# Optimization experiments

Hardware: AMD Instinct MI355X
Metric: run time of the kernel (lower is better)

The kernel has to match this reference:

```python
import jax, jax.numpy as jnp
import numpy as np

N_NODES = 100000
NUM_APS = 1000
K = 2
IN_F = 32
HID = 64


def _glorot(key, shape):
    fan_in, fan_out = shape[-2], shape[-1]
    lim = (6.0 / (fan_in + fan_out)) ** 0.5
    return jax.random.uniform(key, shape, jnp.float32, -lim, lim)


def setup_inputs() -> dict:
    key = jax.random.key(0)
    ks = jax.random.split(key, 12)
    x = jax.random.normal(ks[0], (N_NODES, IN_F), jnp.float32)
    edge_index = jax.random.randint(ks[1], (2, 1600000), 0, N_NODES, jnp.int32)
    edge_attr = jax.random.uniform(ks[2], (1600000, 1), jnp.float32)
    # TAGConv1: K+1 weight matrices [in, hid] + bias
    w1 = _glorot(ks[3], (K + 1, IN_F, HID))
    b1 = jnp.zeros((HID,), jnp.float32)
    # TAGConv2: K+1 weight matrices [hid, hid] + bias
    w2 = _glorot(ks[4], (K + 1, HID, HID))
    b2 = jnp.zeros((HID,), jnp.float32)
    wch = _glorot(ks[5], (HID, 3))
    bch = jnp.zeros((3,), jnp.float32)
    wpw = _glorot(ks[6], (HID, 3))
    bpw = jnp.zeros((3,), jnp.float32)
    return {"x": x, "edge_index": edge_index, "edge_attr": edge_attr,
            "w1": w1, "b1": b1, "w2": w2, "b2": b2,
            "wch": wch, "bch": bch, "wpw": wpw, "bpw": bpw}


def _gcn_norm(edge_index, edge_weight, num_nodes):
    # PyG gcn_norm with add_self_loops=False (TAGConv default)
    row, col = edge_index[0], edge_index[1]
    deg = jax.ops.segment_sum(edge_weight, col, num_segments=num_nodes)
    dinv = jnp.where(deg > 0, deg ** -0.5, 0.0)
    return dinv[row] * edge_weight * dinv[col]


def _tagconv(x, edge_index, norm, w, b):
    # out = sum_k lin_k(A_hat^k x) + b
    row, col = edge_index[0], edge_index[1]
    out = x @ w[0]
    h = x
    for k in range(1, w.shape[0]):
        msg = h[row] * norm[:, None]              # [E, F] gather + scale
        h = jax.ops.segment_sum(msg, col, num_segments=x.shape[0])
        out = out + h @ w[k]
    return out + b


def reference(x, edge_index, edge_attr, w1, b1, w2, b2, wch, bch, wpw, bpw):
    edge_weight = edge_attr.squeeze()
    norm = _gcn_norm(edge_index, edge_weight, x.shape[0])
    h = jax.nn.leaky_relu(_tagconv(x, edge_index, norm, w1, b1), 0.01)
    h = jax.nn.leaky_relu(_tagconv(h, edge_index, norm, w2, b2), 0.01)
    ap = h[:NUM_APS]
    channel_logits = ap @ wch + bch
    power_logits = ap @ wpw + bpw
    return (channel_logits, power_logits)
```

## Files before the change

kernel.cpp:

```cpp
#include <hip/hip_runtime.h>
#include <hip/hip_bf16.h>

#define N_NODES 100000
#define NUM_APS 1000
#define IN_F 32
#define HID 64
#define NB 391
#define EPB 4096
#define CAPB 4608
#define LISTCAP 24000
#define ZERON 100513

typedef __hip_bfloat16 bf16;
typedef unsigned long long ull;
typedef __attribute__((ext_vector_type(8))) short bf16x8;
typedef __attribute__((ext_vector_type(4))) float f32x4;

__device__ __forceinline__ float b2f(bf16 v) { return __bfloat162float(v); }
__device__ __forceinline__ float blo(unsigned u) { return __uint_as_float(u << 16); }
__device__ __forceinline__ float bhi(unsigned u) { return __uint_as_float(u & 0xffff0000u); }
__device__ __forceinline__ unsigned packbf(float x, float y) {
    bf16 a = __float2bfloat16(x), b = __float2bfloat16(y);
    unsigned short ua = *reinterpret_cast<unsigned short*>(&a);
    unsigned short ub = *reinterpret_cast<unsigned short*>(&b);
    return (unsigned)ua | ((unsigned)ub << 16);
}
__device__ __forceinline__ short f2bs(float v) {
    bf16 t = __float2bfloat16(v);
    return *reinterpret_cast<short*>(&t);
}
__device__ __forceinline__ unsigned rec_r(unsigned v) { return v >> 15; }
__device__ __forceinline__ float rec_w(unsigned v) { return (v & 32767u) * (1.f / 32768.f); }

__global__ void zero_k(int* __restrict__ p) {
    int i = blockIdx.x * 256 + threadIdx.x;
    if (i < ZERON) p[i] = 0;
}

__global__ __launch_bounds__(512) void binwrite2_k(const int* __restrict__ row,
                                                   const int* __restrict__ col,
                                                   const float* __restrict__ ew,
                                                   int* __restrict__ binPtr,
                                                   ull* __restrict__ staging, int E) {
    __shared__ int h1[NB];
    __shared__ int base[NB];
    __shared__ int h2[NB];
    for (int i = threadIdx.x; i < NB; i += 512) { h1[i] = 0; h2[i] = 0; }
    __syncthreads();
    int e0 = blockIdx.x * EPB, e1 = min(e0 + EPB, E);
    for (int e = e0 + threadIdx.x; e < e1; e += 512) atomicAdd(&h1[col[e] >> 8], 1);
    __syncthreads();
    for (int i = threadIdx.x; i < NB; i += 512) {
        int v = h1[i];
        base[i] = v ? atomicAdd(&binPtr[i], v) : 0;
    }
    __syncthreads();
    for (int e = e0 + threadIdx.x; e < e1; e += 512) {
        int c = col[e];
        int b = c >> 8;
        int slot = atomicAdd(&h2[b], 1);
        unsigned q = (unsigned)(ew[e] * 32768.0f + 0.5f);
        if (q > 32767u) q = 32767u;
        ull rec = ((ull)(unsigned)(c & 255) << 32) |
                  (ull)(((unsigned)row[e] << 15) | q);
        int pos = base[b] + slot;
        if (pos < CAPB) staging[(size_t)b * CAPB + pos] = rec;
    }
}

__global__ __launch_bounds__(512) void binscan2_k(const int* __restrict__ binPtr,
                                                  int* __restrict__ binBase) {
    __shared__ int s[512];
    int v = (threadIdx.x < NB) ? min(binPtr[threadIdx.x], CAPB) : 0;
    s[threadIdx.x] = v;
    __syncthreads();
    for (int d = 1; d < 512; d <<= 1) {
        int t = (threadIdx.x >= d) ? s[threadIdx.x - d] : 0;
        __syncthreads();
        s[threadIdx.x] += t;
        __syncthreads();
    }
    if (threadIdx.x <= NB) binBase[threadIdx.x] = s[threadIdx.x] - v;
}

__global__ __launch_bounds__(256) void binfin2x_k(const ull* __restrict__ staging,
                                                  const int* __restrict__ binBase,
                                                  const float* __restrict__ x,
                                                  unsigned* __restrict__ ed,
                                                  int* __restrict__ off,
                                                  float* __restrict__ dinv,
                                                  unsigned* __restrict__ xs) {
    __shared__ unsigned cnt[256];
    __shared__ unsigned degq[256];
    __shared__ int wptr[256];
    __shared__ unsigned s[256];
    __shared__ float sdv[256];
    int b = blockIdx.x;
    int e0 = binBase[b];
    int cntb = binBase[b + 1] - e0;
    const ull* st = staging + (size_t)b * CAPB;
    cnt[threadIdx.x] = 0;
    degq[threadIdx.x] = 0;
    __syncthreads();
    for (int i = threadIdx.x; i < cntb; i += 256) {
        ull rec = st[i];
        unsigned cl = (unsigned)(rec >> 32) & 255u;
        atomicAdd(&cnt[cl], 1u);
        atomicAdd(&degq[cl], (unsigned)rec & 32767u);
    }
    __syncthreads();
    unsigned v = cnt[threadIdx.x];
    s[threadIdx.x] = v;
    __syncthreads();
    for (int d = 1; d < 256; d <<= 1) {
        unsigned t = (threadIdx.x >= d) ? s[threadIdx.x - d] : 0;
        __syncthreads();
        s[threadIdx.x] += t;
        __syncthreads();
    }
    int colg = (b << 8) + threadIdx.x;
    float dv = 0.f;
    if (colg < N_NODES) {
        off[colg] = e0 + (int)s[threadIdx.x];
        float deg = (float)degq[threadIdx.x] * (1.0f / 32768.0f);
        dv = deg > 0.f ? 1.0f / sqrtf(deg) : 0.f;
        dinv[colg] = dv;
    }
    sdv[threadIdx.x] = dv;
    wptr[threadIdx.x] = e0 + (int)s[threadIdx.x] - (int)v;
    __syncthreads();
    for (int i = threadIdx.x; i < cntb; i += 256) {
        ull rec = st[i];
        unsigned cl = (unsigned)(rec >> 32) & 255u;
        int pos = atomicAdd(&wptr[cl], 1);
        ed[pos] = (unsigned)rec;
    }
    int nb0 = b << 8;
    for (int idx = threadIdx.x; idx < 256 * 16; idx += 256) {
        int n = idx >> 4, c = idx & 15;
        int gn = nb0 + n;
        if (gn >= N_NODES) break;
        float d = sdv[n];
        xs[(size_t)gn * 16 + c] = packbf(x[(size_t)gn * 32 + 2 * c] * d,
                                         x[(size_t)gn * 32 + 2 * c + 1] * d);
    }
}

__global__ __launch_bounds__(256) void activeset_k(const unsigned* __restrict__ ed,
                                                   const int* __restrict__ off,
                                                   int* __restrict__ mark,
                                                   int* __restrict__ list,
                                                   int* __restrict__ cnt) {
    int e = blockIdx.x * 256 + threadIdx.x;
    int end = off[NUM_APS - 1];
    if (e >= end) return;
    int r = (int)rec_r(ed[e]);
    if (atomicExch(&mark[r], 1) == 0) {
        int pos = atomicAdd(cnt, 1);
        if (pos < LISTCAP) list[pos] = r;
    }
}

__global__ __launch_bounds__(256) void gath32_dual_k(const unsigned* __restrict__ ed,
                                                     const int* __restrict__ off,
                                                     const float* __restrict__ dinv,
                                                     const uint4* __restrict__ src4,
                                                     uint4* __restrict__ p4,
                                                     uint4* __restrict__ u4, int nn) {
    int t = blockIdx.x * 256 + threadIdx.x;
    int n = t >> 2;
    if (n >= nn) return;
    int qd = t & 3;
    int s = (n == 0) ? 0 : off[n - 1];
    int e = off[n];
    float aA[8] = {0,0,0,0,0,0,0,0};
    float aB[8] = {0,0,0,0,0,0,0,0};
    float aC[8] = {0,0,0,0,0,0,0,0};
    float aD[8] = {0,0,0,0,0,0,0,0};
    int i = s;
    for (; i + 4 <= e; i += 4) {
        unsigned v0 = ed[i], v1 = ed[i + 1], v2 = ed[i + 2], v3 = ed[i + 3];
        uint4 s0 = src4[rec_r(v0) * 4 + qd];
        uint4 s1 = src4[rec_r(v1) * 4 + qd];
        uint4 s2 = src4[rec_r(v2) * 4 + qd];
        uint4 s3 = src4[rec_r(v3) * 4 + qd];
        float w0 = rec_w(v0), w1 = rec_w(v1), w2 = rec_w(v2), w3 = rec_w(v3);
        aA[0] += w0 * blo(s0.x); aA[1] += w0 * bhi(s0.x);
        aA[2] += w0 * blo(s0.y); aA[3] += w0 * bhi(s0.y);
        aA[4] += w0 * blo(s0.z); aA[5] += w0 * bhi(s0.z);
        aA[6] += w0 * blo(s0.w); aA[7] += w0 * bhi(s0.w);
        aB[0] += w1 * blo(s1.x); aB[1] += w1 * bhi(s1.x);
        aB[2] += w1 * blo(s1.y); aB[3] += w1 * bhi(s1.y);
        aB[4] += w1 * blo(s1.z); aB[5] += w1 * bhi(s1.z);
        aB[6] += w1 * blo(s1.w); aB[7] += w1 * bhi(s1.w);
        aC[0] += w2 * blo(s2.x); aC[1] += w2 * bhi(s2.x);
        aC[2] += w2 * blo(s2.y); aC[3] += w2 * bhi(s2.y);
        aC[4] += w2 * blo(s2.z); aC[5] += w2 * bhi(s2.z);
        aC[6] += w2 * blo(s2.w); aC[7] += w2 * bhi(s2.w);
        aD[0] += w3 * blo(s3.x); aD[1] += w3 * bhi(s3.x);
        aD[2] += w3 * blo(s3.y); aD[3] += w3 * bhi(s3.y);
        aD[4] += w3 * blo(s3.z); aD[5] += w3 * bhi(s3.z);
        aD[6] += w3 * blo(s3.w); aD[7] += w3 * bhi(s3.w);
    }
    for (; i < e; ++i) {
        unsigned v = ed[i];
        uint4 sv = src4[rec_r(v) * 4 + qd];
        float w = rec_w(v);
        aA[0] += w * blo(sv.x); aA[1] += w * bhi(sv.x);
        aA[2] += w * blo(sv.y); aA[3] += w * bhi(sv.y);
        aA[4] += w * blo(sv.z); aA[5] += w * bhi(sv.z);
        aA[6] += w * blo(sv.w); aA[7] += w * bhi(sv.w);
    }
#pragma unroll
    for (int k = 0; k < 8; ++k) aA[k] += aB[k] + aC[k] + aD[k];
    float d = dinv[n], d2 = d * d;
    p4[n * 4 + qd] = make_uint4(packbf(d * aA[0], d * aA[1]), packbf(d * aA[2], d * aA[3]),
                                packbf(d * aA[4], d * aA[5]), packbf(d * aA[6], d * aA[7]));
    u4[n * 4 + qd] = make_uint4(packbf(d2 * aA[0], d2 * aA[1]), packbf(d2 * aA[2], d2 * aA[3]),
                                packbf(d2 * aA[4], d2 * aA[5]), packbf(d2 * aA[6], d2 * aA[7]));
}

__global__ __launch_bounds__(256) void gath32_one_k(const unsigned* __restrict__ ed,
                                                    const int* __restrict__ off,
                                                    const float* __restrict__ dinv,
                                                    const uint4* __restrict__ src4,
                                                    uint4* __restrict__ p4, int nn) {
    int t = blockIdx.x * 256 + threadIdx.x;
    int n = t >> 2;
    if (n >= nn) return;
    int qd = t & 3;
    int s = (n == 0) ? 0 : off[n - 1];
    int e = off[n];
    float aA[8] = {0,0,0,0,0,0,0,0};
    float aB[8] = {0,0,0,0,0,0,0,0};
    float aC[8] = {0,0,0,0,0,0,0,0};
    float aD[8] = {0,0,0,0,0,0,0,0};
    int i = s;
    for (; i + 4 <= e; i += 4) {
        unsigned v0 = ed[i], v1 = ed[i + 1], v2 = ed[i + 2], v3 = ed[i + 3];
        uint4 s0 = src4[rec_r(v0) * 4 + qd];
        uint4 s1 = src4[rec_r(v1) * 4 + qd];
        uint4 s2 = src4[rec_r(v2) * 4 + qd];
        uint4 s3 = src4[rec_r(v3) * 4 + qd];
        float w0 = rec_w(v0), w1 = rec_w(v1), w2 = rec_w(v2), w3 = rec_w(v3);
        aA[0] += w0 * blo(s0.x); aA[1] += w0 * bhi(s0.x);
        aA[2] += w0 * blo(s0.y); aA[3] += w0 * bhi(s0.y);
        aA[4] += w0 * blo(s0.z); aA[5] += w0 * bhi(s0.z);
        aA[6] += w0 * blo(s0.w); aA[7] += w0 * bhi(s0.w);
        aB[0] += w1 * blo(s1.x); aB[1] += w1 * bhi(s1.x);
        aB[2] += w1 * blo(s1.y); aB[3] += w1 * bhi(s1.y);
        aB[4] += w1 * blo(s1.z); aB[5] += w1 * bhi(s1.z);
        aB[6] += w1 * blo(s1.w); aB[7] += w1 * bhi(s1.w);
        aC[0] += w2 * blo(s2.x); aC[1] += w2 * bhi(s2.x);
        aC[2] += w2 * blo(s2.y); aC[3] += w2 * bhi(s2.y);
        aC[4] += w2 * blo(s2.z); aC[5] += w2 * bhi(s2.z);
        aC[6] += w2 * blo(s2.w); aC[7] += w2 * bhi(s2.w);
        aD[0] += w3 * blo(s3.x); aD[1] += w3 * bhi(s3.x);
        aD[2] += w3 * blo(s3.y); aD[3] += w3 * bhi(s3.y);
        aD[4] += w3 * blo(s3.z); aD[5] += w3 * bhi(s3.z);
        aD[6] += w3 * blo(s3.w); aD[7] += w3 * bhi(s3.w);
    }
    for (; i < e; ++i) {
        unsigned v = ed[i];
        uint4 sv = src4[rec_r(v) * 4 + qd];
        float w = rec_w(v);
        aA[0] += w * blo(sv.x); aA[1] += w * bhi(sv.x);
        aA[2] += w * blo(sv.y); aA[3] += w * bhi(sv.y);
        aA[4] += w * blo(sv.z); aA[5] += w * bhi(sv.z);
        aA[6] += w * blo(sv.w); aA[7] += w * bhi(sv.w);
    }
#pragma unroll
    for (int k = 0; k < 8; ++k) aA[k] += aB[k] + aC[k] + aD[k];
    float d = dinv[n];
    p4[n * 4 + qd] = make_uint4(packbf(d * aA[0], d * aA[1]), packbf(d * aA[2], d * aA[3]),
                                packbf(d * aA[4], d * aA[5]), packbf(d * aA[6], d * aA[7]));
}

__global__ __launch_bounds__(256) void gath64_l2_k(const unsigned* __restrict__ ed,
                                                   const int* __restrict__ off,
                                                   const float* __restrict__ dinv,
                                                   const unsigned* __restrict__ src,
                                                   const int* __restrict__ list,
                                                   const int* __restrict__ cnt,
                                                   unsigned* __restrict__ u,
                                                   unsigned* __restrict__ q) {
    int t = blockIdx.x * 256 + threadIdx.x;
    int idx = t >> 5;
    int fp = t & 31;
    int n;
    bool wq;
    if (idx < NUM_APS) {
        n = idx;
        wq = true;
    } else {
        int j = idx - NUM_APS;
        int c = *cnt;
        if (c > LISTCAP) c = LISTCAP;
        if (j >= c) return;
        n = list[j];
        wq = false;
    }
    int s = (n == 0) ? 0 : off[n - 1];
    int e = off[n];
    float a0 = 0.f, a1 = 0.f, b0 = 0.f, b1 = 0.f;
    int i = s;
    for (; i + 4 <= e; i += 4) {
        unsigned v0 = ed[i], v1 = ed[i + 1], v2 = ed[i + 2], v3 = ed[i + 3];
        unsigned s0 = src[rec_r(v0) * 32 + fp];
        unsigned s1 = src[rec_r(v1) * 32 + fp];
        unsigned s2 = src[rec_r(v2) * 32 + fp];
        unsigned s3 = src[rec_r(v3) * 32 + fp];
        float w0 = rec_w(v0), w1 = rec_w(v1), w2 = rec_w(v2), w3 = rec_w(v3);
        a0 += w0 * blo(s0); a1 += w0 * bhi(s0);
        b0 += w1 * blo(s1); b1 += w1 * bhi(s1);
        a0 += w2 * blo(s2); a1 += w2 * bhi(s2);
        b0 += w3 * blo(s3); b1 += w3 * bhi(s3);
    }
    for (; i < e; ++i) {
        unsigned v = ed[i];
        unsigned sv = src[rec_r(v) * 32 + fp];
        float w = rec_w(v);
        a0 += w * blo(sv); a1 += w * bhi(sv);
    }
    a0 += b0; a1 += b1;
    float d = dinv[n], d2 = d * d;
    u[n * 32 + fp] = packbf(d2 * a0, d2 * a1);
    if (wq) q[n * 32 + fp] = packbf(d * a0, d * a1);
}

__global__ __launch_bounds__(256) void gath64_one_k(const unsigned* __restrict__ ed,
                                                    const int* __restrict__ off,
                                                    const float* __restrict__ dinv,
                                                    const unsigned* __restrict__ src,
                                                    unsigned* __restrict__ q, int nn) {
    int t = blockIdx.x * 256 + threadIdx.x;
    int n = t >> 5;
    if (n >= nn) return;
    int fp = t & 31;
    int s = (n == 0) ? 0 : off[n - 1];
    int e = off[n];
    float a0 = 0.f, a1 = 0.f, b0 = 0.f, b1 = 0.f;
    int i = s;
    for (; i + 4 <= e; i += 4) {
        unsigned v0 = ed[i], v1 = ed[i + 1], v2 = ed[i + 2], v3 = ed[i + 3];
        unsigned s0 = src[rec_r(v0) * 32 + fp];
        unsigned s1 = src[rec_r(v1) * 32 + fp];
        unsigned s2 = src[rec_r(v2) * 32 + fp];
        unsigned s3 = src[rec_r(v3) * 32 + fp];
        float w0 = rec_w(v0), w1 = rec_w(v1), w2 = rec_w(v2), w3 = rec_w(v3);
        a0 += w0 * blo(s0); a1 += w0 * bhi(s0);
        b0 += w1 * blo(s1); b1 += w1 * bhi(s1);
        a0 += w2 * blo(s2); a1 += w2 * bhi(s2);
        b0 += w3 * blo(s3); b1 += w3 * bhi(s3);
    }
    for (; i < e; ++i) {
        unsigned v = ed[i];
        unsigned sv = src[rec_r(v) * 32 + fp];
        float w = rec_w(v);
        a0 += w * blo(sv); a1 += w * bhi(sv);
    }
    a0 += b0; a1 += b1;
    float d = dinv[n];
    q[n * 32 + fp] = packbf(d * a0, d * a1);
}

__global__ __launch_bounds__(256) void dense1m_k(const float* __restrict__ x,
                                                 const unsigned* __restrict__ p1,
                                                 const unsigned* __restrict__ p2,
                                                 const float* __restrict__ w,
                                                 const float* __restrict__ b,
                                                 const float* __restrict__ dinv,
                                                 bf16* __restrict__ h1s,
                                                 bf16* __restrict__ h1p) {
    __shared__ short sxb[64 * 104];
    __shared__ short swt[64 * 104];
    __shared__ float sbias[64];
    __shared__ float sdv[64];
    int tid = threadIdx.x;
    int nb = blockIdx.x * 64;
    for (int idx = tid; idx < 96 * 64; idx += 256) {
        int j = idx >> 6, f = idx & 63;
        swt[f * 104 + j] = f2bs(w[idx]);
    }
    for (int i = tid; i < 64 * 16; i += 256) {
        int n = i >> 4, c = i & 15;
        int gn = nb + n;
        float v0 = 0.f, v1 = 0.f;
        if (gn < N_NODES) {
            v0 = x[(size_t)gn * 32 + 2 * c];
            v1 = x[(size_t)gn * 32 + 2 * c + 1];
        }
        ((unsigned*)sxb)[n * 52 + c] = packbf(v0, v1);
    }
    for (int i = tid; i < 64 * 16; i += 256) {
        int n = i >> 4, c = i & 15;
        int gn = nb + n;
        unsigned v1 = 0u, v2 = 0u;
        if (gn < N_NODES) {
            v1 = p1[(size_t)gn * 16 + c];
            v2 = p2[(size_t)gn * 16 + c];
        }
        ((unsigned*)sxb)[n * 52 + 16 + c] = v1;
        ((unsigned*)sxb)[n * 52 + 32 + c] = v2;
    }
    if (tid < 64) {
        sbias[tid] = b[tid];
        int gn = nb + tid;
        sdv[tid] = (gn < N_NODES) ? dinv[gn] : 0.f;
    }
    __syncthreads();

    int lane = tid & 63;
    int wt = tid >> 6;
    int lr = lane & 15;
    int kg = lane >> 4;
    const short* arow = &sxb[(wt * 16 + lr) * 104 + kg * 8];
    bf16x8 a0 = *(const bf16x8*)(arow);
    bf16x8 a1 = *(const bf16x8*)(arow + 32);
    bf16x8 a2 = *(const bf16x8*)(arow + 64);
#pragma unroll
    for (int ct = 0; ct < 4; ++ct) {
        const short* bcol = &swt[(ct * 16 + lr) * 104 + kg * 8];
        bf16x8 b0 = *(const bf16x8*)(bcol);
        bf16x8 b1 = *(const bf16x8*)(bcol + 32);
        bf16x8 b2 = *(const bf16x8*)(bcol + 64);
        f32x4 acc = {0.f, 0.f, 0.f, 0.f};
        acc = __builtin_amdgcn_mfma_f32_16x16x32_bf16(a0, b0, acc, 0, 0, 0);
        acc = __builtin_amdgcn_mfma_f32_16x16x32_bf16(a1, b1, acc, 0, 0, 0);
        acc = __builtin_amdgcn_mfma_f32_16x16x32_bf16(a2, b2, acc, 0, 0, 0);
        int colo = ct * 16 + lr;
        float bias = sbias[colo];
#pragma unroll
        for (int r = 0; r < 4; ++r) {
            int rowl = wt * 16 + kg * 4 + r;
            int gn = nb + rowl;
            if (gn < N_NODES) {
                float a = acc[r] + bias;
                a = a > 0.f ? a : 0.01f * a;
                h1s[(size_t)gn * HID + colo] = __float2bfloat16(a * sdv[rowl]);
                if (gn < NUM_APS) h1p[(size_t)gn * HID + colo] = __float2bfloat16(a);
            }
        }
    }
}

__global__ __launch_bounds__(256) void dense2l_k(const bf16* __restrict__ h1p,
                                                 const bf16* __restrict__ q1,
                                                 const bf16* __restrict__ q2,
                                                 const float* __restrict__ w,
                                                 const float* __restrict__ b,
                                                 const float* __restrict__ wch,
                                                 const float* __restrict__ bch,
                                                 const float* __restrict__ wpw,
                                                 const float* __restrict__ bpw,
                                                 float* __restrict__ out) {
    __shared__ float sw[3 * HID * HID];
    __shared__ float sx[4][3 * HID];
    __shared__ float sap[4][HID];
    for (int i = threadIdx.x; i < 3 * HID * HID; i += 256) sw[i] = w[i];
    int nb = blockIdx.x * 4;
    for (int k = threadIdx.x; k < 4 * 192; k += 256) {
        int ln = k / 192, j = k % 192;
        int n = nb + ln;
        float v = 0.f;
        if (n < NUM_APS) {
            int hop = j >> 6, ii = j & 63;
            const bf16* sp = (hop == 0) ? h1p : (hop == 1 ? q1 : q2);
            v = b2f(sp[n * HID + ii]);
        }
        sx[ln][j] = v;
    }
    __syncthreads();
    int ln = threadIdx.x >> 6;
    int f = threadIdx.x & 63;
    float acc = b[f];
#pragma unroll 8
    for (int j = 0; j < 192; ++j) acc += sx[ln][j] * sw[j * HID + f];
    acc = acc > 0.f ? acc : 0.01f * acc;
    sap[ln][f] = acc;
    __syncthreads();
    if (threadIdx.x < 24) {
        int lnn = threadIdx.x / 6, j = threadIdx.x % 6;
        int n = nb + lnn;
        if (n < NUM_APS) {
            const float* wp;
            float bb;
            float* o;
            if (j < 3) {
                wp = wch + j; bb = bch[j]; o = out + n * 3 + j;
            } else {
                int jj = j - 3;
                wp = wpw + jj; bb = bpw[jj]; o = out + NUM_APS * 3 + n * 3 + jj;
            }
            float a = bb;
#pragma unroll
            for (int i = 0; i < HID; ++i) a += sap[lnn][i] * wp[i * 3];
            *o = a;
        }
    }
}

extern "C" void kernel_launch(void* const* d_in, const int* in_sizes, int n_in,
                              void* d_out, int out_size, void* d_ws, size_t ws_size,
                              hipStream_t stream) {
    const float* x   = (const float*)d_in[0];
    const int*   ei  = (const int*)d_in[1];
    const float* ea  = (const float*)d_in[2];
    const float* w1  = (const float*)d_in[3];
    const float* b1  = (const float*)d_in[4];
    const float* w2  = (const float*)d_in[5];
    const float* b2  = (const float*)d_in[6];
    const float* wch = (const float*)d_in[7];
    const float* bch = (const float*)d_in[8];
    const float* wpw = (const float*)d_in[9];
    const float* bpw = (const float*)d_in[10];

    const int E = in_sizes[2];
    const int* row  = ei;
    const int* colv = ei + E;

    float* ws = (float*)d_ws;
    ull*      staging = (ull*)ws;
    unsigned* ed      = (unsigned*)(ws + 3700000);
    int*      binPtr  = (int*)(ws + 5300000);
    int*      acnt    = (int*)(ws + 5300512);
    int*      mark    = (int*)(ws + 5300513);
    int*      binBase = (int*)(ws + 5401024);
    int*      off     = (int*)(ws + 5402048);
    float*    dinv    = ws + 5502048;
    unsigned* xs      = (unsigned*)(ws + 5602048);
    unsigned* u1      = xs + 1600000;
    unsigned* p1      = (unsigned*)(ws + 8802048);
    unsigned* p2      = p1 + 1600000;
    unsigned* h1s     = xs;
    unsigned* u3      = p1;
    bf16*     h1p     = (bf16*)(ws + 12002048);
    bf16*     q1      = (bf16*)(ws + 12034048);
    bf16*     q2      = (bf16*)(ws + 12066048);
    int*      alist   = (int*)(ws + 12098048);

    const int gridE = (E + EPB - 1) / EPB;

    zero_k<<<(ZERON + 255) / 256, 256, 0, stream>>>(binPtr);

    binwrite2_k<<<gridE, 512, 0, stream>>>(row, colv, ea, binPtr, staging, E);
    binscan2_k<<<1, 512, 0, stream>>>(binPtr, binBase);
    binfin2x_k<<<NB, 256, 0, stream>>>(staging, binBase, x, ed, off, dinv, xs);

    activeset_k<<<128, 256, 0, stream>>>(ed, off, mark, alist, acnt);

    gath32_dual_k<<<(N_NODES * 4 + 255) / 256, 256, 0, stream>>>(ed, off, dinv,
                                                                 (const uint4*)xs,
                                                                 (uint4*)p1, (uint4*)u1,
                                                                 N_NODES);
    gath32_one_k<<<(N_NODES * 4 + 255) / 256, 256, 0, stream>>>(ed, off, dinv,
                                                                (const uint4*)u1,
                                                                (uint4*)p2, N_NODES);
    dense1m_k<<<(N_NODES + 63) / 64, 256, 0, stream>>>(x, p1, p2, w1, b1, dinv,
                                                       (bf16*)h1s, h1p);

    gath64_l2_k<<<((NUM_APS + LISTCAP) * 32 + 255) / 256, 256, 0, stream>>>(
        ed, off, dinv, h1s, alist, acnt, u3, (unsigned*)q1);
    gath64_one_k<<<(NUM_APS * 32 + 255) / 256, 256, 0, stream>>>(ed, off, dinv, u3,
                                                                 (unsigned*)q2, NUM_APS);
    dense2l_k<<<(NUM_APS + 3) / 4, 256, 0, stream>>>(h1p, q1, q2, w2, b2,
                                                     wch, bch, wpw, bpw, (float*)d_out);
}
```

Baseline: 148.4 us.

## Fuse bin scan, active-set and final gather kernels to cut launches

Removes the single-block bin scan by having each finalize block compute its own prefix offset with a reduction over bin counts. It folds the active-set marking into extra blocks of the first 32-wide gather kernel. It also merges the last hop-2 gather into the final dense kernel. Together these remove three kernel launches and the serialization between them, at the cost of redundant prefix work in every block and a serial per-edge gather loop inside the dense kernel.

```diff
diff --git a/kernel.cpp b/kernel.cpp
--- a/kernel.cpp
+++ b/kernel.cpp
@@ -10,6 +10,8 @@
 #define CAPB 4608
 #define LISTCAP 24000
 #define ZERON 100513
+#define G32 ((N_NODES * 4 + 255) / 256)
+#define ACTB 128
 
 typedef __hip_bfloat16 bf16;
 typedef unsigned long long ull;
@@ -68,75 +70,74 @@
     }
 }
 
-__global__ __launch_bounds__(512) void binscan2_k(const int* __restrict__ binPtr,
-                                                  int* __restrict__ binBase) {
-    __shared__ int s[512];
-    int v = (threadIdx.x < NB) ? min(binPtr[threadIdx.x], CAPB) : 0;
-    s[threadIdx.x] = v;
-    __syncthreads();
-    for (int d = 1; d < 512; d <<= 1) {
-        int t = (threadIdx.x >= d) ? s[threadIdx.x - d] : 0;
-        __syncthreads();
-        s[threadIdx.x] += t;
-        __syncthreads();
-    }
-    if (threadIdx.x <= NB) binBase[threadIdx.x] = s[threadIdx.x] - v;
-}
-
-__global__ __launch_bounds__(256) void binfin2x_k(const ull* __restrict__ staging,
-                                                  const int* __restrict__ binBase,
-                                                  const float* __restrict__ x,
-                                                  unsigned* __restrict__ ed,
-                                                  int* __restrict__ off,
-                                                  float* __restrict__ dinv,
-                                                  unsigned* __restrict__ xs) {
+__global__ __launch_bounds__(256) void binfin3_k(const ull* __restrict__ staging,
+                                                 const int* __restrict__ binPtr,
+                                                 const float* __restrict__ x,
+                                                 unsigned* __restrict__ ed,
+                                                 int* __restrict__ off,
+                                                 float* __restrict__ dinv,
+                                                 unsigned* __restrict__ xs) {
+    __shared__ int sbp[NB];
     __shared__ unsigned cnt[256];
     __shared__ unsigned degq[256];
     __shared__ int wptr[256];
     __shared__ unsigned s[256];
     __shared__ float sdv[256];
+    __shared__ int se0;
     int b = blockIdx.x;
-    int e0 = binBase[b];
-    int cntb = binBase[b + 1] - e0;
+    int tid = threadIdx.x;
+    for (int i = tid; i < NB; i += 256) sbp[i] = min(binPtr[i], CAPB);
+    cnt[tid] = 0;
+    degq[tid] = 0;
+    __syncthreads();
+    int partial = 0;
+    for (int i = tid; i < b; i += 256) partial += sbp[i];
+    s[tid] = (unsigned)partial;
+    __syncthreads();
+    for (int d = 128; d > 0; d >>= 1) {
+        if (tid < d) s[tid] += s[tid + d];
+        __syncthreads();
+    }
+    if (tid == 0) se0 = (int)s[0];
+    __syncthreads();
+    int e0 = se0;
+    int cntb = sbp[b];
     const ull* st = staging + (size_t)b * CAPB;
-    cnt[threadIdx.x] = 0;
-    degq[threadIdx.x] = 0;
-    __syncthreads();
-    for (int i = threadIdx.x; i < cntb; i += 256) {
+    for (int i = tid; i < cntb; i += 256) {
         ull rec = st[i];
         unsigned cl = (unsigned)(rec >> 32) & 255u;
         atomicAdd(&cnt[cl], 1u);
         atomicAdd(&degq[cl], (unsigned)rec & 32767u);
     }
     __syncthreads();
-    unsigned v = cnt[threadIdx.x];
-    s[threadIdx.x] = v;
+    unsigned v = cnt[tid];
+    s[tid] = v;
     __syncthreads();
     for (int d = 1; d < 256; d <<= 1) {
-        unsigned t = (threadIdx.x >= d) ? s[threadIdx.x - d] : 0;
+        unsigned t = (tid >= d) ? s[tid - d] : 0;
         __syncthreads();
-        s[threadIdx.x] += t;
+        s[tid] += t;
         __syncthreads();
     }
-    int colg = (b << 8) + threadIdx.x;
+    int colg = (b << 8) + tid;
     float dv = 0.f;
     if (colg < N_NODES) {
-        off[colg] = e0 + (int)s[threadIdx.x];
-        float deg = (float)degq[threadIdx.x] * (1.0f / 32768.0f);
+        off[colg] = e0 + (int)s[tid];
+        float deg = (float)degq[tid] * (1.0f / 32768.0f);
         dv = deg > 0.f ? 1.0f / sqrtf(deg) : 0.f;
         dinv[colg] = dv;
     }
-    sdv[threadIdx.x] = dv;
-    wptr[threadIdx.x] = e0 + (int)s[threadIdx.x] - (int)v;
-    __syncthreads();
-    for (int i = threadIdx.x; i < cntb; i += 256) {
+    sdv[tid] = dv;
+    wptr[tid] = e0 + (int)s[tid] - (int)v;
+    __syncthreads();
+    for (int i = tid; i < cntb; i += 256) {
         ull rec = st[i];
         unsigned cl = (unsigned)(rec >> 32) & 255u;
         int pos = atomicAdd(&wptr[cl], 1);
         ed[pos] = (unsigned)rec;
     }
     int nb0 = b << 8;
-    for (int idx = threadIdx.x; idx < 256 * 16; idx += 256) {
+    for (int idx = tid; idx < 256 * 16; idx += 256) {
         int n = idx >> 4, c = idx & 15;
         int gn = nb0 + n;
         if (gn >= N_NODES) break;
@@ -146,30 +147,30 @@
     }
 }
 
-__global__ __launch_bounds__(256) void activeset_k(const unsigned* __restrict__ ed,
-                                                   const int* __restrict__ off,
-                                                   int* __restrict__ mark,
-                                                   int* __restrict__ list,
-                                                   int* __restrict__ cnt) {
-    int e = blockIdx.x * 256 + threadIdx.x;
-    int end = off[NUM_APS - 1];
-    if (e >= end) return;
-    int r = (int)rec_r(ed[e]);
-    if (atomicExch(&mark[r], 1) == 0) {
-        int pos = atomicAdd(cnt, 1);
-        if (pos < LISTCAP) list[pos] = r;
-    }
-}
-
-__global__ __launch_bounds__(256) void gath32_dual_k(const unsigned* __restrict__ ed,
-                                                     const int* __restrict__ off,
-                                                     const float* __restrict__ dinv,
-                                                     const uint4* __restrict__ src4,
-                                                     uint4* __restrict__ p4,
-                                                     uint4* __restrict__ u4, int nn) {
+__global__ __launch_bounds__(256) void gath32a_k(const unsigned* __restrict__ ed,
+                                                 const int* __restrict__ off,
+                                                 const float* __restrict__ dinv,
+                                                 const uint4* __restrict__ src4,
+                                                 uint4* __restrict__ p4,
+                                                 uint4* __restrict__ u4,
+                                                 int* __restrict__ mark,
+                                                 int* __restrict__ list,
+                                                 int* __restrict__ cnt) {
+    if (blockIdx.x >= G32) {
+        int e = (blockIdx.x - G32) * 256 + threadIdx.x;
+        int end = off[NUM_APS - 1];
+        if (e < end) {
+            int r = (int)rec_r(ed[e]);
+            if (atomicExch(&mark[r], 1) == 0) {
+                int pos = atomicAdd(cnt, 1);
+                if (pos < LISTCAP) list[pos] = r;
+            }
+        }
+        return;
+    }
     int t = blockIdx.x * 256 + threadIdx.x;
     int n = t >> 2;
-    if (n >= nn) return;
+    if (n >= N_NODES) return;
     int qd = t & 3;
     int s = (n == 0) ? 0 : off[n - 1];
     int e = off[n];
@@ -328,42 +329,6 @@
     if (wq) q[n * 32 + fp] = packbf(d * a0, d * a1);
 }
 
-__global__ __launch_bounds__(256) void gath64_one_k(const unsigned* __restrict__ ed,
-                                                    const int* __restrict__ off,
-                                                    const float* __restrict__ dinv,
-                                                    const unsigned* __restrict__ src,
-                                                    unsigned* __restrict__ q, int nn) {
-    int t = blockIdx.x * 256 + threadIdx.x;
-    int n = t >> 5;
-    if (n >= nn) return;
-    int fp = t & 31;
-    int s = (n == 0) ? 0 : off[n - 1];
-    int e = off[n];
-    float a0 = 0.f, a1 = 0.f, b0 = 0.f, b1 = 0.f;
-    int i = s;
-    for (; i + 4 <= e; i += 4) {
-        unsigned v0 = ed[i], v1 = ed[i + 1], v2 = ed[i + 2], v3 = ed[i + 3];
-        unsigned s0 = src[rec_r(v0) * 32 + fp];
-        unsigned s1 = src[rec_r(v1) * 32 + fp];
-        unsigned s2 = src[rec_r(v2) * 32 + fp];
-        unsigned s3 = src[rec_r(v3) * 32 + fp];
-        float w0 = rec_w(v0), w1 = rec_w(v1), w2 = rec_w(v2), w3 = rec_w(v3);
-        a0 += w0 * blo(s0); a1 += w0 * bhi(s0);
-        b0 += w1 * blo(s1); b1 += w1 * bhi(s1);
-        a0 += w2 * blo(s2); a1 += w2 * bhi(s2);
-        b0 += w3 * blo(s3); b1 += w3 * bhi(s3);
-    }
-    for (; i < e; ++i) {
-        unsigned v = ed[i];
-        unsigned sv = src[rec_r(v) * 32 + fp];
-        float w = rec_w(v);
-        a0 += w * blo(sv); a1 += w * bhi(sv);
-    }
-    a0 += b0; a1 += b1;
-    float d = dinv[n];
-    q[n * 32 + fp] = packbf(d * a0, d * a1);
-}
-
 __global__ __launch_bounds__(256) void dense1m_k(const float* __restrict__ x,
                                                  const unsigned* __restrict__ p1,
                                                  const unsigned* __restrict__ p2,
@@ -444,9 +409,12 @@
     }
 }
 
-__global__ __launch_bounds__(256) void dense2l_k(const bf16* __restrict__ h1p,
+__global__ __launch_bounds__(256) void dense2g_k(const bf16* __restrict__ h1p,
                                                  const bf16* __restrict__ q1,
-                                                 const bf16* __restrict__ q2,
+                                                 const unsigned* __restrict__ u3,
+                                                 const unsigned* __restrict__ ed,
+                                                 const int* __restrict__ off,
+                                                 const float* __restrict__ dinv,
                                                  const float* __restrict__ w,
                                                  const float* __restrict__ b,
                                                  const float* __restrict__ wch,
@@ -457,46 +425,61 @@
     __shared__ float sw[3 * HID * HID];
     __shared__ float sx[4][3 * HID];
     __shared__ float sap[4][HID];
-    for (int i = threadIdx.x; i < 3 * HID * HID; i += 256) sw[i] = w[i];
+    int tid = threadIdx.x;
+    for (int i = tid; i < 3 * HID * HID; i += 256) sw[i] = w[i];
     int nb = blockIdx.x * 4;
-    for (int k = threadIdx.x; k < 4 * 192; k += 256) {
-        int ln = k / 192, j = k % 192;
+    for (int k = tid; k < 4 * 128; k += 256) {
+        int ln = k >> 7, j = k & 127;
         int n = nb + ln;
-        float v = 0.f;
-        if (n < NUM_APS) {
-            int hop = j >> 6, ii = j & 63;
-            const bf16* sp = (hop == 0) ? h1p : (hop == 1 ? q1 : q2);
-            v = b2f(sp[n * HID + ii]);
+        const bf16* sp = (j < 64) ? h1p : q1;
+        sx[ln][j] = b2f(sp[n * HID + (j & 63)]);
+    }
+    {
+        int ln = tid >> 6;
+        int half = tid & 63;
+        if (half < 32) {
+            int n = nb + ln;
+            int fp = half;
+            int s0 = (n == 0) ? 0 : off[n - 1];
+            int e = off[n];
+            float a0 = 0.f, a1 = 0.f;
+            for (int i = s0; i < e; ++i) {
+                unsigned v = ed[i];
+                unsigned sv = u3[rec_r(v) * 32 + fp];
+                float wq = rec_w(v);
+                a0 += wq * blo(sv);
+                a1 += wq * bhi(sv);
+            }
+            float d = dinv[n];
+            sx[ln][128 + 2 * fp]     = d * a0;
+            sx[ln][128 + 2 * fp + 1] = d * a1;
         }
-        sx[ln][j] = v;
-    }
-    __syncthreads();
-    int ln = threadIdx.x >> 6;
-    int f = threadIdx.x & 63;
+    }
+    __syncthreads();
+    int ln = tid >> 6;
+    int f = tid & 63;
     float acc = b[f];
 #pragma unroll 8
     for (int j = 0; j < 192; ++j) acc += sx[ln][j] * sw[j * HID + f];
     acc = acc > 0.f ? acc : 0.01f * acc;
     sap[ln][f] = acc;
     __syncthreads();
-    if (threadIdx.x < 24) {
-        int lnn = threadIdx.x / 6, j = threadIdx.x % 6;
+    if (tid < 24) {
+        int lnn = tid / 6, j = tid % 6;
         int n = nb + lnn;
-        if (n < NUM_APS) {
-            const float* wp;
-            float bb;
-            float* o;
-            if (j < 3) {
-                wp = wch + j; bb = bch[j]; o = out + n * 3 + j;
-            } else {
-                int jj = j - 3;
-                wp = wpw + jj; bb = bpw[jj]; o = out + NUM_APS * 3 + n * 3 + jj;
-            }
-            float a = bb;
+        const float* wp;
+        float bb;
+        float* o;
+        if (j < 3) {
+            wp = wch + j; bb = bch[j]; o = out + n * 3 + j;
+        } else {
+            int jj = j - 3;
+            wp = wpw + jj; bb = bpw[jj]; o = out + NUM_APS * 3 + n * 3 + jj;
+        }
+        float a = bb;
 #pragma unroll
-            for (int i = 0; i < HID; ++i) a += sap[lnn][i] * wp[i * 3];
-            *o = a;
-        }
+        for (int i = 0; i < HID; ++i) a += sap[lnn][i] * wp[i * 3];
+        *o = a;
     }
 }
 
@@ -525,7 +508,6 @@
     int*      binPtr  = (int*)(ws + 5300000);
     int*      acnt    = (int*)(ws + 5300512);
     int*      mark    = (int*)(ws + 5300513);
-    int*      binBase = (int*)(ws + 5401024);
     int*      off     = (int*)(ws + 5402048);
     float*    dinv    = ws + 5502048;
     unsigned* xs      = (unsigned*)(ws + 5602048);
@@ -536,7 +518,6 @@
     unsigned* u3      = p1;
     bf16*     h1p     = (bf16*)(ws + 12002048);
     bf16*     q1      = (bf16*)(ws + 12034048);
-    bf16*     q2      = (bf16*)(ws + 12066048);
     int*      alist   = (int*)(ws + 12098048);
 
     const int gridE = (E + EPB - 1) / EPB;
@@ -544,15 +525,11 @@
     zero_k<<<(ZERON + 255) / 256, 256, 0, stream>>>(binPtr);
 
     binwrite2_k<<<gridE, 512, 0, stream>>>(row, colv, ea, binPtr, staging, E);
-    binscan2_k<<<1, 512, 0, stream>>>(binPtr, binBase);
-    binfin2x_k<<<NB, 256, 0, stream>>>(staging, binBase, x, ed, off, dinv, xs);
-
-    activeset_k<<<128, 256, 0, stream>>>(ed, off, mark, alist, acnt);
-
-    gath32_dual_k<<<(N_NODES * 4 + 255) / 256, 256, 0, stream>>>(ed, off, dinv,
-                                                                 (const uint4*)xs,
-                                                                 (uint4*)p1, (uint4*)u1,
-                                                                 N_NODES);
+    binfin3_k<<<NB, 256, 0, stream>>>(staging, binPtr, x, ed, off, dinv, xs);
+
+    gath32a_k<<<G32 + ACTB, 256, 0, stream>>>(ed, off, dinv, (const uint4*)xs,
+                                              (uint4*)p1, (uint4*)u1,
+                                              mark, alist, acnt);
     gath32_one_k<<<(N_NODES * 4 + 255) / 256, 256, 0, stream>>>(ed, off, dinv,
                                                                 (const uint4*)u1,
                                                                 (uint4*)p2, N_NODES);
@@ -561,8 +538,6 @@
 
     gath64_l2_k<<<((NUM_APS + LISTCAP) * 32 + 255) / 256, 256, 0, stream>>>(
         ed, off, dinv, h1s, alist, acnt, u3, (unsigned*)q1);
-    gath64_one_k<<<(NUM_APS * 32 + 255) / 256, 256, 0, stream>>>(ed, off, dinv, u3,
-                                                                 (unsigned*)q2, NUM_APS);
-    dense2l_k<<<(NUM_APS + 3) / 4, 256, 0, stream>>>(h1p, q1, q2, w2, b2,
-                                                     wch, bch, wpw, bpw, (float*)d_out);
-}
+    dense2g_k<<<NUM_APS / 4, 256, 0, stream>>>(h1p, q1, u3, ed, off, dinv, w2, b2,
+                                               wch, bch, wpw, bpw, (float*)d_out);
+}
```

Result: no change. 149.2 us (+0.5%).
